# Kernel optimization log

Measured on AMD Instinct MI355X. Metric: run time of the kernel, lower is better.

Reference implementation:

```python
import jax, jax.numpy as jnp
import numpy as np
import math

NUM_HEADS = 8
EPS = 1e-5
LEAKY_SLOPE = 0.01


def _attention(q, k, v, mask):
    # q:[S,64] k,v:[T,64] -> [S,64]; scale by sqrt(d) per source (q.shape[1])
    s = (q @ k.T) / math.sqrt(q.shape[1])
    if mask:
        S, T = s.shape
        tri = jnp.tril(jnp.ones((S, T), dtype=bool))
        s = jnp.where(tri, s, -jnp.inf)
    return jax.nn.softmax(s, axis=1) @ v


def _mha(q, k, v, w_o, mask):
    # all heads share the same (q,k,v) in the source, so cat over heads == tile
    head = _attention(q, k, v, mask)            # [S,64]
    concat = jnp.tile(head, (1, NUM_HEADS))     # [S,512]
    return concat @ w_o


def _layernorm(x, g, b):
    mu = jnp.mean(x, axis=-1, keepdims=True)
    var = jnp.var(x, axis=-1, keepdims=True)
    return (x - mu) * jax.lax.rsqrt(var + EPS) * g + b


def setup_inputs() -> dict:
    key = jax.random.key(0)
    ks = jax.random.split(key, 12)
    S, D, P, H = 8192, 512, 64, 2048
    sd = 1.0 / math.sqrt(D)
    return {
        "encoder_output": jax.random.normal(ks[0], (S, D), jnp.float32),
        "previous_stage_output": jax.random.normal(ks[1], (S, D), jnp.float32),
        "wq_m": jax.random.normal(ks[2], (D, P), jnp.float32) * sd,
        "wk_m": jax.random.normal(ks[3], (D, P), jnp.float32) * sd,
        "wv_m": jax.random.normal(ks[4], (D, P), jnp.float32) * sd,
        "wq_c": jax.random.normal(ks[5], (D, P), jnp.float32) * sd,
        "wk_c": jax.random.normal(ks[6], (D, P), jnp.float32) * sd,
        "wv_c": jax.random.normal(ks[7], (D, P), jnp.float32) * sd,
        "w_o": jax.random.normal(ks[8], (D, D), jnp.float32) * sd,
        "ln_g": jnp.ones((D,), jnp.float32),
        "ln_b": jnp.zeros((D,), jnp.float32),
        "w1": jax.random.normal(ks[9], (D, H), jnp.float32) * sd,
        "b1": jnp.zeros((H,), jnp.float32),
        "w2": jax.random.normal(ks[10], (H, D), jnp.float32) * (1.0 / math.sqrt(H)),
        "b2": jnp.zeros((D,), jnp.float32),
    }


def reference(encoder_output, previous_stage_output, wq_m, wk_m, wv_m,
              wq_c, wk_c, wv_c, w_o, ln_g, ln_b, w1, b1, w2, b2):
    prev = previous_stage_output
    # masked (causal) self-attention over previous decoder output
    masked_mh = _mha(prev @ wq_m, prev @ wk_m, prev @ wv_m, w_o, mask=True)
    # cross attention: q from masked output, k/v from encoder output
    mh = _mha(masked_mh @ wq_c, encoder_output @ wk_c, encoder_output @ wv_c,
              w_o, mask=False)
    x = _layernorm(mh + prev, ln_g, ln_b)
    h = x @ w1 + b1
    h = jnp.where(h >= 0, h, LEAKY_SLOPE * h)
    ffn = h @ w2 + b2
    out = _layernorm(ffn + x, ln_g, ln_b)
    return (encoder_output, out)
```

## Files before the change

kernel.cpp:

```cpp
#include <hip/hip_runtime.h>
#include <hip/hip_bf16.h>

typedef unsigned short u16;
typedef __attribute__((ext_vector_type(4))) float f32x4;
typedef __attribute__((ext_vector_type(8))) __bf16 bf16x8;
typedef __attribute__((ext_vector_type(8))) short short8;
typedef __attribute__((ext_vector_type(4))) short s16x4;

constexpr int SEQ = 8192;
constexpr int DM  = 512;
constexpr int HD  = 64;
constexpr int HFF = 2048;

__device__ __forceinline__ float b2f(u16 u){
  union { unsigned int i; float f; } v; v.i = ((unsigned int)u) << 16; return v.f;
}
__device__ __forceinline__ u16 f2b(float f){
  union { float f; unsigned int i; } v; v.f = f;
  unsigned int r = v.i + 0x7FFFu + ((v.i >> 16) & 1u);
  return (u16)(r >> 16);
}

__device__ __forceinline__ void gload16(const u16* g, u16* lds){
  __builtin_amdgcn_global_load_lds(
      (const __attribute__((address_space(1))) void*)g,
      (__attribute__((address_space(3))) void*)lds, 16, 0, 0);
}

__global__ __launch_bounds__(256) void copycvt_k(const float* __restrict__ in,
                                                 float* __restrict__ outf,
                                                 u16* __restrict__ outb, long n8){
  long i = blockIdx.x * 256L + threadIdx.x;
  if(i >= n8) return;
  f32x4 a = ((const f32x4*)in)[i*2];
  f32x4 b = ((const f32x4*)in)[i*2+1];
  ((f32x4*)outf)[i*2]   = a;
  ((f32x4*)outf)[i*2+1] = b;
  u16 ov[8];
  for(int j=0;j<4;j++){ ov[j] = f2b(a[j]); ov[4+j] = f2b(b[j]); }
  ((short8*)outb)[i] = *(short8*)ov;
}

__global__ __launch_bounds__(256) void cvt_k(const float* __restrict__ in,
                                             u16* __restrict__ out, long n8){
  long i = blockIdx.x * 256L + threadIdx.x;
  if(i >= n8) return;
  f32x4 a = ((const f32x4*)in)[i*2];
  f32x4 b = ((const f32x4*)in)[i*2+1];
  u16 ov[8];
  for(int j=0;j<4;j++){ ov[j] = f2b(a[j]); ov[4+j] = f2b(b[j]); }
  ((short8*)out)[i] = *(short8*)ov;
}

__global__ __launch_bounds__(256) void wtrans6_k(const float* __restrict__ w0,
                                                 const float* __restrict__ w1,
                                                 const float* __restrict__ w2,
                                                 const float* __restrict__ w3,
                                                 const float* __restrict__ w4,
                                                 const float* __restrict__ w5,
                                                 u16* __restrict__ out){
  __shared__ u16 t[32][33];
  const float* ins[6] = {w0,w1,w2,w3,w4,w5};
  const float* in = ins[blockIdx.z];
  u16* o = out + (long)blockIdx.z * 32768;
  int c0 = blockIdx.x*32, r0 = blockIdx.y*32;
  int tx = threadIdx.x, ty = threadIdx.y;
  for(int i=0;i<4;i++)
    t[ty+i*8][tx] = f2b(in[(long)(r0+ty+i*8)*HD + c0+tx]);
  __syncthreads();
  for(int i=0;i<4;i++) o[(long)(c0+ty+i*8)*DM + r0+tx] = t[tx][ty+i*8];
}

template<int IN_F>
__global__ __launch_bounds__(256) void transpose_k(const void* __restrict__ inp,
                                                   u16* __restrict__ out, int R, int C){
  __shared__ u16 t[32][33];
  int c0 = blockIdx.x*32, r0 = blockIdx.y*32;
  int tx = threadIdx.x, ty = threadIdx.y;
  for(int i=0;i<4;i++){
    long idx = (long)(r0+ty+i*8)*C + c0+tx;
    u16 v;
    if constexpr (IN_F) v = f2b(((const float*)inp)[idx]);
    else                v = ((const u16*)inp)[idx];
    t[ty+i*8][tx] = v;
  }
  __syncthreads();
  for(int i=0;i<4;i++) out[(long)(c0+ty+i*8)*R + r0+tx] = t[tx][ty+i*8];
}

__global__ __launch_bounds__(256) void vtrans2_k(const u16* __restrict__ v0,
                                                 u16* __restrict__ o0,
                                                 const u16* __restrict__ v1,
                                                 u16* __restrict__ o1){
  __shared__ u16 t[32][33];
  const u16* in = blockIdx.z ? v1 : v0;
  u16* o = blockIdx.z ? o1 : o0;
  int c0 = blockIdx.x*32, r0 = blockIdx.y*32;
  int tx = threadIdx.x, ty = threadIdx.y;
  for(int i=0;i<4;i++) t[ty+i*8][tx] = in[(long)(r0+ty+i*8)*HD + c0+tx];
  __syncthreads();
  for(int i=0;i<4;i++) o[(long)(c0+ty+i*8)*SEQ + r0+tx] = t[tx][ty+i*8];
}

__global__ __launch_bounds__(256) void wosum_k(const float* __restrict__ wo,
                                               u16* __restrict__ outT){
  int tid = blockIdx.x*256 + threadIdx.x;
  int n = tid >> 6, p = tid & 63;
  float s = 0.f;
  for(int h=0; h<8; h++) s += wo[(long)(h*64+p)*DM + n];
  outT[n*64+p] = f2b(s);
}

template<bool WRITE_BF>
__global__ __launch_bounds__(256) void add_ln(const u16* __restrict__ Xa,
                                              const float* __restrict__ Xb,
                                              const float* __restrict__ G,
                                              const float* __restrict__ Bb,
                                              float* __restrict__ OutF,
                                              u16* __restrict__ OutB){
  int row  = blockIdx.x*4 + (threadIdx.x>>6);
  int lane = threadIdx.x & 63;
  short8 a8 = *(const short8*)&Xa[(long)row*DM + lane*8];
  f32x4 b0 = *(const f32x4*)&Xb[(long)row*DM + lane*8];
  f32x4 b1 = *(const f32x4*)&Xb[(long)row*DM + lane*8 + 4];
  float x[8]; float s=0.f, s2=0.f;
  for(int i=0;i<8;i++){
    float bv = (i<4) ? b0[i] : b1[i-4];
    x[i] = b2f((u16)a8[i]) + bv;
    s += x[i]; s2 += x[i]*x[i];
  }
  for(int o=1;o<64;o<<=1){ s += __shfl_xor(s,o); s2 += __shfl_xor(s2,o); }
  float mu  = s * (1.f/DM);
  float var = s2 * (1.f/DM) - mu*mu;
  float rstd = rsqrtf(var + 1e-5f);
  f32x4 g0 = *(const f32x4*)&G[lane*8];
  f32x4 g1 = *(const f32x4*)&G[lane*8+4];
  f32x4 p0 = *(const f32x4*)&Bb[lane*8];
  f32x4 p1 = *(const f32x4*)&Bb[lane*8+4];
  float of[8]; u16 ob[8];
  for(int i=0;i<8;i++){
    float gv = (i<4)?g0[i]:g1[i-4], bv2 = (i<4)?p0[i]:p1[i-4];
    float v = (x[i]-mu)*rstd*gv + bv2;
    of[i] = v; ob[i] = f2b(v);
  }
  *(f32x4*)&OutF[(long)row*DM + lane*8]     = *(f32x4*)&of[0];
  *(f32x4*)&OutF[(long)row*DM + lane*8 + 4] = *(f32x4*)&of[4];
  if constexpr (WRITE_BF)
    *(short8*)&OutB[(long)row*DM + lane*8] = *(short8*)ob;
}

template<int BM,int BN,int EPI>
__global__ __launch_bounds__(256) void gemm2(const u16* __restrict__ A,
                                             const u16* __restrict__ Bt,
                                             u16* __restrict__ C,
                                             const float* __restrict__ bias,
                                             int N, int K, long sB, long sC){
  constexpr int WR=2, WC=2;
  constexpr int WM = BM/WR, WN = BN/WC;
  constexpr int MF = WM/16, NF = WN/16;
  __shared__ u16 As[2][BM*64];
  __shared__ u16 Bs[2][BN*64];

  const int tid = threadIdx.x;
  const int wid = tid >> 6, lane = tid & 63;
  const int g = lane >> 4, lr = lane & 15;
  const int m0 = blockIdx.x * BM;
  const int n0 = blockIdx.y * BN;
  Bt += (long)blockIdx.z * sB;
  C  += (long)blockIdx.z * sC;
  const int wr = wid / WC, wc = wid % WC;

  f32x4 acc[MF][NF];
  for(int m=0;m<MF;m++) for(int n=0;n<NF;n++) acc[m][n] = (f32x4)0.f;

  auto stage = [&](const u16* src, int base_row, u16* lds, int rows, int k0){
    const int cpw = rows/32;
    for(int i=0;i<cpw;i++){
      int chunk = wid*cpw + i;
      int Lb = chunk*1024;
      int L  = Lb + lane*16;
      int row = L >> 7, cb = L & 127;
      int scb = cb ^ ((row&7)<<4);
      gload16(&src[(long)(base_row+row)*K + k0 + (scb>>1)], lds + (Lb>>1));
    }
  };

  const int nk = K/64;
  stage(A, m0, As[0], BM, 0);
  stage(Bt, n0, Bs[0], BN, 0);
  __syncthreads();
  int cur = 0;
  for(int t=0;t<nk;t++){
    if(t+1<nk){
      stage(A, m0, As[cur^1], BM, (t+1)*64);
      stage(Bt, n0, Bs[cur^1], BN, (t+1)*64);
    }
    for(int kc=0;kc<2;kc++){
      const int co = (kc*32 + g*8) ^ ((lr&7)<<3);
      bf16x8 af[MF], bfr[NF];
      for(int m=0;m<MF;m++) af[m]  = *(const bf16x8*)&As[cur][(wr*WM+m*16+lr)*64 + co];
      for(int n=0;n<NF;n++) bfr[n] = *(const bf16x8*)&Bs[cur][(wc*WN+n*16+lr)*64 + co];
      for(int m=0;m<MF;m++)
        for(int n=0;n<NF;n++)
          acc[m][n] = __builtin_amdgcn_mfma_f32_16x16x32_bf16(af[m], bfr[n], acc[m][n], 0,0,0);
    }
    __syncthreads();
    cur ^= 1;
  }
  for(int m=0;m<MF;m++){
    int row = m0 + wr*WM + m*16 + g*4;
    for(int n=0;n<NF;n++){
      int col = n0 + wc*WN + n*16 + lr;
      float bv = 0.f;
      if constexpr (EPI>=1) bv = bias[col];
      for(int j=0;j<4;j++){
        float v = acc[m][n][j] + bv;
        if constexpr (EPI==2) v = (v >= 0.f) ? v : 0.01f*v;
        C[(long)(row+j)*N + col] = f2b(v);
      }
    }
  }
}

template<bool CAUSAL>
__global__ __launch_bounds__(256) void attn_part_k(const u16* __restrict__ Q,
                                                   const u16* __restrict__ Km,
                                                   const u16* __restrict__ Vt,
                                                   float* __restrict__ Op,
                                                   float* __restrict__ Ml){
  constexpr int LDP = 72;
  constexpr int NCH = 16;
  constexpr int CTI = 8;
  __shared__ u16 Ks[2][64*64];
  __shared__ u16 Vs[2][64*64];
  __shared__ u16 Ps[4*16*LDP];

  const int qb = blockIdx.x, ci = blockIdx.y;
  if(CAUSAL && ci*CTI > qb) return;

  const int tid = threadIdx.x, wid = tid>>6, lane = tid&63;
  const int g = lane>>4, lr = lane&15, r4 = g*4;
  const int qrow = qb*64 + wid*16;

  const int srow0 = wid*16 + (lane>>3);
  const int scb   = ((lane&7)*16) ^ (((lane>>3)&7)<<4);
  const int sco   = scb>>1;

  auto stageKV = [&](int buf, int kv0){
    for(int i=0;i<2;i++){
      int Lb  = (wid*2+i)*1024;
      int row = srow0 + i*8;
      gload16(&Km[(long)(kv0+row)*HD + sco],     &Ks[buf][Lb>>1]);
      gload16(&Vt[(long)row*SEQ + kv0 + sco],    &Vs[buf][Lb>>1]);
    }
  };

  bf16x8 qf[2];
  for(int kc=0;kc<2;kc++){
    bf16x8 t = *(const bf16x8*)&Q[(long)(qrow + lr)*HD + kc*32 + g*8];
    for(int i=0;i<8;i++) t[i] = (__bf16)((float)t[i] * 0.1803368801f);
    qf[kc] = t;
  }

  f32x4 o[4]; for(int n=0;n<4;n++) o[n] = (f32x4)0.f;
  float mst = -1e30f, lst = 0.f;

  const int tdiag = qb - ci*CTI;
  const int tmax = CAUSAL ? min(CTI, tdiag + 1) : CTI;

  stageKV(0, ci*512);
  __syncthreads();
  int cur = 0;

  for(int t=0; t<tmax; ++t){
    const int kv0 = ci*512 + t*64;
    if(t+1 < tmax) stageKV(cur^1, kv0 + 64);

    f32x4 s[4]; for(int n=0;n<4;n++) s[n] = (f32x4)0.f;
    for(int kc=0;kc<2;kc++){
      const int co = (kc*32 + g*8) ^ ((lr&7)<<3);
      for(int n=0;n<4;n++){
        bf16x8 kf = *(const bf16x8*)&Ks[cur][(n*16+lr)*64 + co];
        s[n] = __builtin_amdgcn_mfma_f32_16x16x32_bf16(kf, qf[kc], s[n], 0,0,0);
      }
    }
    if(CAUSAL && t == tdiag){
      int row = qrow + lr;
      for(int n=0;n<4;n++)
        for(int j=0;j<4;j++)
          if(kv0 + n*16 + r4 + j > row) s[n][j] = -1e30f;
    }
    float pmax = s[0][0];
    for(int n=0;n<4;n++)
      for(int j=0;j<4;j++) pmax = fmaxf(pmax, s[n][j]);
    pmax = fmaxf(pmax, __shfl_xor(pmax,16));
    pmax = fmaxf(pmax, __shfl_xor(pmax,32));
    if(__any(pmax > mst + 8.f)){
      float mn = fmaxf(mst, pmax);
      float fac = exp2f(mst - mn);
      mst = mn; lst *= fac;
      float fj0 = __shfl(fac, r4+0), fj1 = __shfl(fac, r4+1);
      float fj2 = __shfl(fac, r4+2), fj3 = __shfl(fac, r4+3);
      for(int n=0;n<4;n++){
        o[n][0] *= fj0; o[n][1] *= fj1; o[n][2] *= fj2; o[n][3] *= fj3;
      }
    }
    float rs = 0.f;
    for(int n=0;n<4;n++){
      u16 w[4];
      for(int j=0;j<4;j++){
        float p = exp2f(s[n][j] - mst);
        rs += p;
        __bf16 pb = (__bf16)p;
        union { __bf16 b; u16 u; } cv; cv.b = pb;
        w[j] = cv.u;
      }
      *(s16x4*)&Ps[(wid*16 + lr)*LDP + n*16 + r4] = *(s16x4*)w;
    }
    rs += __shfl_xor(rs,16); rs += __shfl_xor(rs,32);
    lst += rs;
    for(int kc=0;kc<2;kc++){
      bf16x8 pf = *(const bf16x8*)&Ps[(wid*16 + lr)*LDP + kc*32 + g*8];
      const int co = (kc*32 + g*8) ^ ((lr&7)<<3);
      for(int n=0;n<4;n++){
        bf16x8 vf = *(const bf16x8*)&Vs[cur][(n*16+lr)*64 + co];
        o[n] = __builtin_amdgcn_mfma_f32_16x16x32_bf16(pf, vf, o[n], 0,0,0);
      }
    }
    __syncthreads();
    cur ^= 1;
  }
  const long pr = (long)(qb*NCH + ci)*64;
  for(int n=0;n<4;n++)
    for(int j=0;j<4;j++)
      Op[(pr + wid*16 + r4 + j)*64 + n*16 + lr] = o[n][j];
  if(lane < 16){
    Ml[(pr + wid*16 + lr)*2]     = mst;
    Ml[(pr + wid*16 + lr)*2 + 1] = lst;
  }
}

template<bool CAUSAL>
__global__ __launch_bounds__(256) void attn_red_k(const float* __restrict__ Op,
                                                  const float* __restrict__ Ml,
                                                  u16* __restrict__ O){
  int r = blockIdx.x*4 + (threadIdx.x>>6);
  int d = threadIdx.x & 63;
  int qb = r >> 6, rt = r & 63;
  int nch = CAUSAL ? (qb>>3) + 1 : 16;
  long base = (long)qb*16*64 + rt;
  float m = -1e30f;
  for(int i=0;i<nch;i++) m = fmaxf(m, Ml[(base + i*64)*2]);
  float L = 0.f, acc = 0.f;
  for(int i=0;i<nch;i++){
    float mi = Ml[(base + i*64)*2], li = Ml[(base + i*64)*2 + 1];
    float w = exp2f(mi - m);
    L   += li * w;
    acc += w * Op[(base + i*64)*64 + d];
  }
  O[(long)r*HD + d] = f2b(acc / L);
}

extern "C" void kernel_launch(void* const* d_in, const int* in_sizes, int n_in,
                              void* d_out, int out_size, void* d_ws, size_t ws_size,
                              hipStream_t stream){
  const float* enc  = (const float*)d_in[0];
  const float* prev = (const float*)d_in[1];
  const float* wq_m = (const float*)d_in[2];
  const float* wk_m = (const float*)d_in[3];
  const float* wv_m = (const float*)d_in[4];
  const float* wq_c = (const float*)d_in[5];
  const float* wk_c = (const float*)d_in[6];
  const float* wv_c = (const float*)d_in[7];
  const float* w_o  = (const float*)d_in[8];
  const float* ln_g = (const float*)d_in[9];
  const float* ln_b = (const float*)d_in[10];
  const float* w1   = (const float*)d_in[11];
  const float* b1   = (const float*)d_in[12];
  const float* w2   = (const float*)d_in[13];
  const float* b2   = (const float*)d_in[14];
  float* out = (float*)d_out;
  u16* ws  = (u16*)d_ws;

  u16* wq_m_t = ws;
  u16* wk_c_t = wq_m_t + 4*32768;
  u16* wost   = wq_m_t + 6*32768;
  u16* w1_t   = wost   + 32768;
  u16* w2_t   = w1_t   + 1048576;
  u16* enc_b  = w2_t   + 1048576;
  u16* prev_b = enc_b  + 4194304;
  u16* q_m    = prev_b + 4194304;
  u16* k_m    = q_m    + 524288;
  u16* v_m    = k_m    + 524288;
  u16* v_m_t  = v_m    + 524288;
  u16* head_m = v_m_t  + 524288;
  u16* k_c    = head_m + 524288;
  u16* v_c    = k_c    + 524288;
  u16* v_c_t  = v_c    + 524288;
  u16* q_c    = v_c_t  + 524288;
  u16* head_c = q_c    + 524288;
  u16* mmh    = head_c + 524288;
  u16* mh     = mmh    + 4194304;
  u16* xb     = mh     + 4194304;
  float* xf   = (float*)(xb + 4194304);
  u16* hbuf   = enc_b;
  u16* ffn    = mh;
  float* Op   = (float*)mmh;
  float* Ml   = Op + (long)128*16*64*64;

  dim3 b256(256), tb(32,8);

  copycvt_k<<<dim3(2048), b256, 0, stream>>>(enc, out, enc_b, (long)SEQ*DM/8);
  cvt_k<<<dim3(2048), b256, 0, stream>>>(prev, prev_b, (long)SEQ*DM/8);

  wtrans6_k<<<dim3(2,16,6), tb, 0, stream>>>(wq_m, wk_m, wv_m, wq_c, wk_c, wv_c, wq_m_t);
  transpose_k<1><<<dim3(64,16), tb, 0, stream>>>(w1, w1_t, DM, HFF);
  transpose_k<1><<<dim3(16,64), tb, 0, stream>>>(w2, w2_t, HFF, DM);
  wosum_k<<<dim3(128), b256, 0, stream>>>(w_o, wost);

  gemm2<64,64,0><<<dim3(SEQ/64,1,3), b256, 0, stream>>>(prev_b, wq_m_t, q_m, nullptr, HD, DM, 32768, 524288);
  gemm2<64,64,0><<<dim3(SEQ/64,1,2), b256, 0, stream>>>(enc_b,  wk_c_t, k_c, nullptr, HD, DM, 32768, 524288);
  vtrans2_k<<<dim3(2,256,2), tb, 0, stream>>>(v_m, v_m_t, v_c, v_c_t);

  attn_part_k<true><<<dim3(SEQ/64, 16), b256, 0, stream>>>(q_m, k_m, v_m_t, Op, Ml);
  attn_red_k<true><<<dim3(SEQ/4), b256, 0, stream>>>(Op, Ml, head_m);
  gemm2<64,128,0><<<dim3(SEQ/64,4,1), b256, 0, stream>>>(head_m, wost, mmh, nullptr, DM, HD, 0, 0);

  gemm2<64,64,0><<<dim3(SEQ/64,1,1), b256, 0, stream>>>(mmh, wq_m_t + 3*32768, q_c, nullptr, HD, DM, 0, 0);
  attn_part_k<false><<<dim3(SEQ/64, 16), b256, 0, stream>>>(q_c, k_c, v_c_t, Op, Ml);
  attn_red_k<false><<<dim3(SEQ/4), b256, 0, stream>>>(Op, Ml, head_c);
  gemm2<64,128,0><<<dim3(SEQ/64,4,1), b256, 0, stream>>>(head_c, wost, mh, nullptr, DM, HD, 0, 0);

  add_ln<true><<<dim3(SEQ/4), b256, 0, stream>>>(mh, prev, ln_g, ln_b, xf, xb);

  gemm2<128,128,2><<<dim3(SEQ/128,HFF/128,1), b256, 0, stream>>>(xb, w1_t, hbuf, b1, HFF, DM, 0, 0);
  gemm2<64,128,1><<<dim3(SEQ/64,4,1),         b256, 0, stream>>>(hbuf, w2_t, ffn, b2, DM, HFF, 0, 0);

  add_ln<false><<<dim3(SEQ/4), b256, 0, stream>>>(ffn, xf, ln_g, ln_b, out + (long)SEQ*DM, nullptr);
}
```

Measured before the change: 228.0 us.

## Load K/V fragments directly from global memory instead of LDS double-buffering

The attention partial kernel drops its shared-memory double-buffered K/V staging and the per-tile block barrier. Each wave now loads its K and V^T MFMA fragments straight from global memory into registers, relying on L2/L1 for reuse across the four waves. The V loads are issued early so they overlap the softmax work. This removes LDS traffic and __syncthreads, at the cost of roughly four times more global/L1 load traffic, uncoalesced strided V^T reads, and higher register pressure.

```diff
diff --git a/kernel.cpp b/kernel.cpp
--- a/kernel.cpp
+++ b/kernel.cpp
@@ -231,8 +231,6 @@
   constexpr int LDP = 72;
   constexpr int NCH = 16;
   constexpr int CTI = 8;
-  __shared__ u16 Ks[2][64*64];
-  __shared__ u16 Vs[2][64*64];
   __shared__ u16 Ps[4*16*LDP];
 
   const int qb = blockIdx.x, ci = blockIdx.y;
@@ -241,19 +239,6 @@
   const int tid = threadIdx.x, wid = tid>>6, lane = tid&63;
   const int g = lane>>4, lr = lane&15, r4 = g*4;
   const int qrow = qb*64 + wid*16;
-
-  const int srow0 = wid*16 + (lane>>3);
-  const int scb   = ((lane&7)*16) ^ (((lane>>3)&7)<<4);
-  const int sco   = scb>>1;
-
-  auto stageKV = [&](int buf, int kv0){
-    for(int i=0;i<2;i++){
-      int Lb  = (wid*2+i)*1024;
-      int row = srow0 + i*8;
-      gload16(&Km[(long)(kv0+row)*HD + sco],     &Ks[buf][Lb>>1]);
-      gload16(&Vt[(long)row*SEQ + kv0 + sco],    &Vs[buf][Lb>>1]);
-    }
-  };
 
   bf16x8 qf[2];
   for(int kc=0;kc<2;kc++){
@@ -268,31 +253,33 @@
   const int tdiag = qb - ci*CTI;
   const int tmax = CAUSAL ? min(CTI, tdiag + 1) : CTI;
 
-  stageKV(0, ci*512);
-  __syncthreads();
-  int cur = 0;
-
   for(int t=0; t<tmax; ++t){
     const int kv0 = ci*512 + t*64;
-    if(t+1 < tmax) stageKV(cur^1, kv0 + 64);
 
     f32x4 s[4]; for(int n=0;n<4;n++) s[n] = (f32x4)0.f;
-    for(int kc=0;kc<2;kc++){
-      const int co = (kc*32 + g*8) ^ ((lr&7)<<3);
-      for(int n=0;n<4;n++){
-        bf16x8 kf = *(const bf16x8*)&Ks[cur][(n*16+lr)*64 + co];
-        s[n] = __builtin_amdgcn_mfma_f32_16x16x32_bf16(kf, qf[kc], s[n], 0,0,0);
-      }
-    }
+    {
+      bf16x8 kf[2][4];
+      for(int n=0;n<4;n++)
+        for(int kc=0;kc<2;kc++)
+          kf[kc][n] = *(const bf16x8*)&Km[(long)(kv0 + n*16 + lr)*HD + kc*32 + g*8];
+      for(int kc=0;kc<2;kc++)
+        for(int n=0;n<4;n++)
+          s[n] = __builtin_amdgcn_mfma_f32_16x16x32_bf16(kf[kc][n], qf[kc], s[n], 0,0,0);
+    }
+    bf16x8 vfr[2][4];
+    for(int n=0;n<4;n++)
+      for(int kc=0;kc<2;kc++)
+        vfr[kc][n] = *(const bf16x8*)&Vt[(long)(n*16 + lr)*SEQ + kv0 + kc*32 + g*8];
+
     if(CAUSAL && t == tdiag){
       int row = qrow + lr;
       for(int n=0;n<4;n++)
         for(int j=0;j<4;j++)
           if(kv0 + n*16 + r4 + j > row) s[n][j] = -1e30f;
     }
-    float pmax = s[0][0];
-    for(int n=0;n<4;n++)
-      for(int j=0;j<4;j++) pmax = fmaxf(pmax, s[n][j]);
+    f32x4 mv = s[0];
+    for(int j=0;j<4;j++) mv[j] = fmaxf(fmaxf(s[0][j],s[1][j]), fmaxf(s[2][j],s[3][j]));
+    float pmax = fmaxf(fmaxf(mv[0],mv[1]), fmaxf(mv[2],mv[3]));
     pmax = fmaxf(pmax, __shfl_xor(pmax,16));
     pmax = fmaxf(pmax, __shfl_xor(pmax,32));
     if(__any(pmax > mst + 8.f)){
@@ -321,14 +308,9 @@
     lst += rs;
     for(int kc=0;kc<2;kc++){
       bf16x8 pf = *(const bf16x8*)&Ps[(wid*16 + lr)*LDP + kc*32 + g*8];
-      const int co = (kc*32 + g*8) ^ ((lr&7)<<3);
-      for(int n=0;n<4;n++){
-        bf16x8 vf = *(const bf16x8*)&Vs[cur][(n*16+lr)*64 + co];
-        o[n] = __builtin_amdgcn_mfma_f32_16x16x32_bf16(pf, vf, o[n], 0,0,0);
-      }
-    }
-    __syncthreads();
-    cur ^= 1;
+      for(int n=0;n<4;n++)
+        o[n] = __builtin_amdgcn_mfma_f32_16x16x32_bf16(pf, vfr[kc][n], o[n], 0,0,0);
+    }
   }
   const long pr = (long)(qb*NCH + ci)*64;
   for(int n=0;n<4;n++)
```

Result: slower. 357.4 us (+56.8%).
